# Performance work log

Measured on AMD Instinct MI355X. Metric: run time of the kernel, lower is better.

Reference implementation:

```python
import jax, jax.numpy as jnp
import numpy as np

SCALE = 0.25  # LoRA alpha / rank


def setup_inputs() -> dict:
    N, K, E, H, D, R = 1024, 2, 16, 1024, 2048, 16
    key = jax.random.key(0)
    ks = jax.random.split(key, 9)
    hidden_states = jax.random.normal(ks[0], (N, D), jnp.float32)
    topk_weights = jax.random.uniform(ks[1], (N, K), jnp.float32)
    topk_weights = topk_weights / topk_weights.sum(-1, keepdims=True)
    topk_ids = jax.random.randint(ks[2], (N, K), 0, E, jnp.int32)
    w_up = jax.random.normal(ks[3], (E, 2 * H, D), jnp.float32) * 0.02
    w_down = jax.random.normal(ks[4], (E, D, H), jnp.float32) * 0.02
    up_a = jax.random.normal(ks[5], (E, R, D), jnp.float32) * 0.02
    up_b = jax.random.normal(ks[6], (E, 2 * H, R), jnp.float32) * 0.02
    down_a = jax.random.normal(ks[7], (E, R, H), jnp.float32) * 0.02
    down_b = jax.random.normal(ks[8], (E, D, R), jnp.float32) * 0.02
    return {
        'hidden_states': hidden_states,
        'topk_weights': topk_weights,
        'topk_ids': topk_ids,
        'w_up': w_up,
        'w_down': w_down,
        'up_a': up_a,
        'up_b': up_b,
        'down_a': down_a,
        'down_b': down_b,
    }


def reference(hidden_states, topk_weights, topk_ids, w_up, w_down, up_a, up_b, down_a, down_b):
    H = w_down.shape[2]  # hidden_size
    # Up projection: dense per-expert GEMM, then gather the selected expert per (token, k).
    up_dense = jnp.einsum('nd,eod->neo', hidden_states, w_up)          # [N, E, 2H]
    up = jnp.take_along_axis(up_dense, topk_ids[:, :, None], axis=1)   # [N, K, 2H]
    # LoRA on up-proj: out[:, k] += (x @ A_e.T @ B_e.T) * scale
    t = jnp.einsum('nd,nkrd->nkr', hidden_states, up_a[topk_ids])      # [N, K, R]
    up = up + SCALE * jnp.einsum('nkr,nkor->nko', t, up_b[topk_ids])   # [N, K, 2H]
    # fused_gelu_and_mul: gelu(first half) * second half (erf gelu)
    act = jax.nn.gelu(up[..., :H], approximate=False) * up[..., H:]    # [N, K, H]
    # Down projection with routed-weight multiply.
    down_dense = jnp.einsum('nkh,edh->nked', act, w_down)              # [N, K, E, D]
    down = jnp.take_along_axis(down_dense, topk_ids[:, :, None, None], axis=2)[:, :, 0, :]  # [N, K, D]
    # LoRA on down-proj (topk_weights applied to lora path too, matching _apply_moe_lora)
    t2 = jnp.einsum('nkh,nkrh->nkr', act, down_a[topk_ids])            # [N, K, R]
    ldown = jnp.einsum('nkr,nkdr->nkd', t2, down_b[topk_ids])          # [N, K, D]
    down = (down + SCALE * ldown) * topk_weights[:, :, None]
    # moe_sum: reduce over top_k
    return down.sum(axis=1)                                            # [N, D]
```

## Files before the change

kernel.cpp:

```cpp
#include <hip/hip_runtime.h>
#include <math.h>

#define N_TOK 1024
#define TOPK  2
#define NEXP  16
#define HID   1024
#define DIM   2048
#define RANK  16
#define NPAIR (N_TOK * TOPK)
#define MOE_SCALE 0.25f
#define MAXTILES 31

typedef __attribute__((ext_vector_type(8))) short short8;
typedef __attribute__((ext_vector_type(4))) float floatx4;

static __device__ __forceinline__ unsigned short f2bf(float f) {
    union { float f; unsigned int u; } v; v.f = f;
    unsigned int u = v.u;
    u += 0x7fffu + ((u >> 16) & 1u);
    return (unsigned short)(u >> 16);
}

static __device__ __forceinline__ short8 cvt8(float4 a, float4 b) {
    short8 o;
    o[0] = (short)f2bf(a.x); o[1] = (short)f2bf(a.y);
    o[2] = (short)f2bf(a.z); o[3] = (short)f2bf(a.w);
    o[4] = (short)f2bf(b.x); o[5] = (short)f2bf(b.y);
    o[6] = (short)f2bf(b.z); o[7] = (short)f2bf(b.w);
    return o;
}

#define BAR() do { asm volatile("s_waitcnt lgkmcnt(0)" ::: "memory"); \
                   __builtin_amdgcn_s_barrier(); } while (0)

__global__ void k_routing(const int* __restrict__ ids,
                          int* __restrict__ offs,
                          int* __restrict__ sorted,
                          int* __restrict__ tlist,
                          int* __restrict__ tcount) {
    __shared__ int s_cnt[NEXP];
    __shared__ int s_off[NEXP + 1];
    int tid = threadIdx.x;
    if (tid < NEXP) s_cnt[tid] = 0;
    __syncthreads();
    for (int p = tid; p < NPAIR; p += blockDim.x) atomicAdd(&s_cnt[ids[p]], 1);
    __syncthreads();
    if (tid == 0) {
        int acc = 0;
        for (int e = 0; e < NEXP; ++e) { s_off[e] = acc; acc += s_cnt[e]; }
        s_off[NEXP] = acc;
        int t = 0;
        for (int e = 0; e < NEXP; ++e) {
            int c = s_off[e + 1] - s_off[e];
            for (int m = 0; m * 128 < c; ++m) tlist[t++] = (e << 8) | m;
        }
        *tcount = t;
    }
    __syncthreads();
    if (tid <= NEXP) offs[tid] = s_off[tid];
    if (tid < NEXP) s_cnt[tid] = s_off[tid];
    __syncthreads();
    for (int p = tid; p < NPAIR; p += blockDim.x) {
        int e = ids[p];
        int slot = atomicAdd(&s_cnt[e], 1);
        sorted[slot] = p;
    }
}

__global__ void k_cvt_x(const float* __restrict__ x, unsigned short* __restrict__ xbf) {
    size_t i = (size_t)blockIdx.x * blockDim.x + threadIdx.x;
    const float4* p = (const float4*)(x + i * 8);
    float4 a = p[0], b = p[1];
    *(short8*)(xbf + i * 8) = cvt8(a, b);
}

#define G_ISSUE(c, RA, RB, RU) do {                                          \
    const unsigned short* _a = aptr + (size_t)(c) * 64;                      \
    const float* _b = bptr + (size_t)(c) * 64;                               \
    _Pragma("unroll") for (int j = 0; j < 4; ++j)                            \
        RA[j] = *(const short8*)(_a + 8 * j);                                \
    _Pragma("unroll") for (int j = 0; j < 8; ++j)                            \
        RB[j] = *(const float4*)(_b + 4 * j);                                \
    if (tid < 128) {                                                         \
        const float* _u = uptr + (size_t)(c) * 64;                           \
        RU[0] = *(const float4*)_u;                                          \
        RU[1] = *(const float4*)(_u + 4);                                    \
    }                                                                        \
} while (0)

#define G_WRITE(RA, RB, RU, BUF) do {                                        \
    _Pragma("unroll") for (int cc = 0; cc < 4; ++cc) {                       \
        int cl = (tid & 1) * 4 + cc;                                         \
        *(short8*)(&sA[BUF][row * 64 + ((cl ^ (row & 7)) * 8)]) = RA[cc];    \
        short8 vb = cvt8(RB[2 * cc], RB[2 * cc + 1]);                        \
        *(short8*)(&sB[BUF][row * 64 + ((cl ^ (row & 7)) * 8)]) = vb;        \
    }                                                                        \
    if (tid < 128) {                                                         \
        short8 vu = cvt8(RU[0], RU[1]);                                      \
        int cl = tid & 7;                                                    \
        *(short8*)(&sU[BUF][urow * 64 + ((cl ^ (urow & 7)) * 8)]) = vu;      \
    }                                                                        \
} while (0)

#define G_MSTEP(BUF) do {                                                    \
    _Pragma("unroll") for (int kk = 0; kk < 2; ++kk) {                       \
        int r0 = wv * 32 + lm, r1 = wv * 32 + 16 + lm;                       \
        short8 af0 = *(const short8*)(&sA[BUF][r0 * 64 + (((kk * 4 + lq) ^ (r0 & 7)) * 8)]); \
        short8 af1 = *(const short8*)(&sA[BUF][r1 * 64 + (((kk * 4 + lq) ^ (r1 & 7)) * 8)]); \
        short8 uf  = *(const short8*)(&sU[BUF][lm * 64 + (((kk * 4 + lq) ^ (lm & 7)) * 8)]); \
        acct[0] = __builtin_amdgcn_mfma_f32_16x16x32_bf16(af0, uf, acct[0], 0, 0, 0); \
        acct[1] = __builtin_amdgcn_mfma_f32_16x16x32_bf16(af1, uf, acct[1], 0, 0, 0); \
        _Pragma("unroll") for (int n2 = 0; n2 < 8; ++n2) {                   \
            int rr = n2 * 16 + lm;                                           \
            short8 bf = *(const short8*)(&sB[BUF][rr * 64 + (((kk * 4 + lq) ^ (rr & 7)) * 8)]); \
            acc[0][n2] = __builtin_amdgcn_mfma_f32_16x16x32_bf16(af0, bf, acc[0][n2], 0, 0, 0); \
            acc[1][n2] = __builtin_amdgcn_mfma_f32_16x16x32_bf16(af1, bf, acc[1][n2], 0, 0, 0); \
        }                                                                    \
    }                                                                        \
} while (0)

#define G_PIPE(NC)                                                           \
    G_ISSUE(0, ra0, rb0, ru0);                                               \
    G_ISSUE(1, ra1, rb1, ru1);                                               \
    G_WRITE(ra0, rb0, ru0, 0);                                               \
    G_ISSUE(2, ra0, rb0, ru0);                                               \
    BAR();                                                                   \
    _Pragma("unroll 1")                                                      \
    for (int kc = 0; kc < (NC); kc += 2) {                                   \
        G_MSTEP(0);                                                          \
        G_WRITE(ra1, rb1, ru1, 1);                                           \
        if (kc + 3 < (NC)) G_ISSUE(kc + 3, ra1, rb1, ru1);                   \
        BAR();                                                               \
        G_MSTEP(1);                                                          \
        if (kc + 2 < (NC)) G_WRITE(ra0, rb0, ru0, 0);                        \
        if (kc + 4 < (NC)) G_ISSUE(kc + 4, ra0, rb0, ru0);                   \
        BAR();                                                               \
    }

__global__ __launch_bounds__(256, 2) void k_up(
        const unsigned short* __restrict__ xbf, const float* __restrict__ w_up,
        const float* __restrict__ up_a, const float* __restrict__ up_b,
        const int* __restrict__ offs, const int* __restrict__ sorted,
        const int* __restrict__ tlist, const int* __restrict__ tcount,
        unsigned short* __restrict__ act) {
    int wt = blockIdx.x;
    if (wt >= *tcount) return;
    int code = tlist[wt];
    int e = code >> 8, mt = code & 255;
    int nt = blockIdx.y;
    int off = offs[e], cnt = offs[e + 1] - off;

    __shared__ __align__(16) unsigned short sA[2][128 * 64];
    __shared__ __align__(16) unsigned short sB[2][128 * 64];
    __shared__ __align__(16) unsigned short sU[2][16 * 64];

    int tid = threadIdx.x, lane = tid & 63, wv = tid >> 6;
    int lm = lane & 15, lq = lane >> 4;

    int row  = tid >> 1;
    int colh = (tid & 1) * 32;

    int g = mt * 128 + row; if (g >= cnt) g = cnt - 1;
    int p = sorted[off + g];
    const unsigned short* aptr = xbf + (size_t)(p >> 1) * DIM + colh;

    int wrow = (row < 64) ? (nt * 64 + row) : (HID + nt * 64 + (row - 64));
    const float* bptr = w_up + ((size_t)e * 2 * HID + wrow) * DIM + colh;

    int urow = (tid >> 3) & 15, ucol = (tid & 7) * 8;
    const float* uptr = up_a + ((size_t)e * RANK + urow) * DIM + ucol;

    floatx4 zero = {0.f, 0.f, 0.f, 0.f};
    floatx4 acc[2][8], acct[2];
#pragma unroll
    for (int i = 0; i < 2; ++i) {
        acct[i] = zero;
#pragma unroll
        for (int j = 0; j < 8; ++j) acc[i][j] = zero;
    }

    short8 ra0[4], ra1[4];
    float4 rb0[8], rb1[8];
    float4 ru0[2], ru1[2];

    G_PIPE(32);

    float* t_s = (float*)&sA[0][0];
#pragma unroll
    for (int i = 0; i < 2; ++i)
#pragma unroll
        for (int j = 0; j < 4; ++j)
            t_s[(wv * 32 + i * 16 + lq * 4 + j) * 16 + lm] = MOE_SCALE * acct[i][j];
    BAR();

    const float* upb = up_b + (size_t)e * 2 * HID * RANK;
#pragma unroll
    for (int n2 = 0; n2 < 4; ++n2) {
        int h = nt * 64 + n2 * 16 + lm;
        const float* b1 = upb + (size_t)h * RANK;
        const float* b2 = upb + (size_t)(h + HID) * RANK;
        float r1[RANK], r2[RANK];
#pragma unroll
        for (int i = 0; i < RANK; ++i) { r1[i] = b1[i]; r2[i] = b2[i]; }
#pragma unroll
        for (int i = 0; i < 2; ++i) {
#pragma unroll
            for (int r = 0; r < 4; ++r) {
                int rl = wv * 32 + i * 16 + lq * 4 + r;
                int gg = mt * 128 + rl;
                if (gg < cnt) {
                    int slot = off + gg;
                    const float* tv = t_s + rl * 16;
                    float s1 = acc[i][n2][r], s2 = acc[i][n2 + 4][r];
#pragma unroll
                    for (int j = 0; j < RANK; ++j) { s1 += tv[j] * r1[j]; s2 += tv[j] * r2[j]; }
                    float gl = 0.5f * s1 * (1.f + erff(s1 * 0.70710678118654752f));
                    act[(size_t)slot * HID + h] = f2bf(gl * s2);
                }
            }
        }
    }
}

__global__ __launch_bounds__(256, 2) void k_down(
        const unsigned short* __restrict__ actg, const float* __restrict__ w_down,
        const float* __restrict__ tw, const float* __restrict__ down_a,
        const float* __restrict__ down_b,
        const int* __restrict__ offs, const int* __restrict__ sorted,
        const int* __restrict__ tlist, const int* __restrict__ tcount,
        float* __restrict__ out) {
    int wt = blockIdx.x;
    if (wt >= *tcount) return;
    int code = tlist[wt];
    int e = code >> 8, mt = code & 255;
    int nt = blockIdx.y;
    int off = offs[e], cnt = offs[e + 1] - off;

    __shared__ __align__(16) unsigned short sA[2][128 * 64];
    __shared__ __align__(16) unsigned short sB[2][128 * 64];
    __shared__ __align__(16) unsigned short sU[2][16 * 64];

    int tid = threadIdx.x, lane = tid & 63, wv = tid >> 6;
    int lm = lane & 15, lq = lane >> 4;

    int row  = tid >> 1;
    int colh = (tid & 1) * 32;

    int g = mt * 128 + row; if (g >= cnt) g = cnt - 1;
    const unsigned short* aptr = actg + (size_t)(off + g) * HID + colh;

    int d = nt * 128 + row;
    const float* bptr = w_down + ((size_t)e * DIM + d) * HID + colh;

    int urow = (tid >> 3) & 15, ucol = (tid & 7) * 8;
    const float* uptr = down_a + ((size_t)e * RANK + urow) * HID + ucol;

    floatx4 zero = {0.f, 0.f, 0.f, 0.f};
    floatx4 acc[2][8], acct[2];
#pragma unroll
    for (int i = 0; i < 2; ++i) {
        acct[i] = zero;
#pragma unroll
        for (int j = 0; j < 8; ++j) acc[i][j] = zero;
    }

    short8 ra0[4], ra1[4];
    float4 rb0[8], rb1[8];
    float4 ru0[2], ru1[2];

    G_PIPE(16);

    float* t_s = (float*)&sA[0][0];
#pragma unroll
    for (int i = 0; i < 2; ++i)
#pragma unroll
        for (int j = 0; j < 4; ++j)
            t_s[(wv * 32 + i * 16 + lq * 4 + j) * 16 + lm] = MOE_SCALE * acct[i][j];
    BAR();

#pragma unroll
    for (int n2 = 0; n2 < 8; ++n2) {
        int dd = nt * 128 + n2 * 16 + lm;
        const float* rb = down_b + ((size_t)e * DIM + dd) * RANK;
        float rbv[RANK];
#pragma unroll
        for (int i2 = 0; i2 < RANK; ++i2) rbv[i2] = rb[i2];
#pragma unroll
        for (int i = 0; i < 2; ++i) {
#pragma unroll
            for (int r = 0; r < 4; ++r) {
                int rl = wv * 32 + i * 16 + lq * 4 + r;
                int gg = mt * 128 + rl;
                if (gg < cnt) {
                    int slot = off + gg;
                    int pp = sorted[slot];
                    const float* tv = t_s + rl * 16;
                    float val = acc[i][n2][r];
#pragma unroll
                    for (int j = 0; j < RANK; ++j) val += tv[j] * rbv[j];
                    atomicAdd(&out[(size_t)(pp >> 1) * DIM + dd], val * tw[pp]);
                }
            }
        }
    }
}

extern "C" void kernel_launch(void* const* d_in, const int* in_sizes, int n_in,
                              void* d_out, int out_size, void* d_ws, size_t ws_size,
                              hipStream_t stream) {
    const float* x      = (const float*)d_in[0];
    const float* tw     = (const float*)d_in[1];
    const int*   ids    = (const int*)d_in[2];
    const float* w_up   = (const float*)d_in[3];
    const float* w_down = (const float*)d_in[4];
    const float* up_a   = (const float*)d_in[5];
    const float* up_b   = (const float*)d_in[6];
    const float* down_a = (const float*)d_in[7];
    const float* down_b = (const float*)d_in[8];
    float* out = (float*)d_out;

    char* ws = (char*)d_ws;
    int* offs   = (int*)ws;
    int* tlist  = (int*)(ws + 1024);
    int* tcount = (int*)(ws + 2048);
    int* sorted = (int*)(ws + 4096);
    unsigned short* act = (unsigned short*)(ws + 65536);
    unsigned short* xbf = (unsigned short*)(ws + 65536 + (size_t)NPAIR * HID * 2);

    hipMemsetAsync(d_out, 0, (size_t)out_size * sizeof(float), stream);

    k_routing<<<1, 256, 0, stream>>>(ids, offs, sorted, tlist, tcount);
    k_cvt_x<<<(N_TOK * DIM / 8 / 256), 256, 0, stream>>>(x, xbf);

    dim3 grid(MAXTILES, 16);
    k_up<<<grid, 256, 0, stream>>>(xbf, w_up, up_a, up_b, offs, sorted, tlist, tcount, act);
    k_down<<<grid, 256, 0, stream>>>(act, w_down, tw, down_a, down_b, offs, sorted, tlist, tcount, out);
}
```

Measured before the change: 603.4 us.

## Stream GEMM tiles into LDS with direct global-to-LDS loads, halve N tile

Replaces the register-staged global loads and LDS writes in both MoE GEMM kernels with direct global_load_lds transfers. Weights are now stored as fp32 in swizzled LDS and converted to bf16 at fragment-read time, and the pipeline waits on vmcnt counters instead of a register double buffer. The N tile shrinks from 128 to 64 columns, so the grid doubles to 32 column blocks. This aims to cut VGPR pressure and issue overhead in the load path. In exchange, each weight fragment is converted on every read, and the activation tile and LoRA-A are reloaded across twice as many blocks.

```diff
diff --git a/kernel.cpp b/kernel.cpp
--- a/kernel.cpp
+++ b/kernel.cpp
@@ -30,8 +30,19 @@
     return o;
 }
 
+static __device__ __forceinline__ short8 ldcvt(const float* base, int r, int c) {
+    float4 f0 = *(const float4*)(base + r * 64 + (((c)     ^ (r & 15)) * 4));
+    float4 f1 = *(const float4*)(base + r * 64 + (((c + 1) ^ (r & 15)) * 4));
+    return cvt8(f0, f1);
+}
+
 #define BAR() do { asm volatile("s_waitcnt lgkmcnt(0)" ::: "memory"); \
-                   __builtin_amdgcn_s_barrier(); } while (0)
+                   __builtin_amdgcn_s_barrier(); \
+                   asm volatile("" ::: "memory"); } while (0)
+
+#define GLDS16(G, L) __builtin_amdgcn_global_load_lds( \
+    (const __attribute__((address_space(1))) void*)(G), \
+    (__attribute__((address_space(3))) void*)(L), 16, 0, 0)
 
 __global__ void k_routing(const int* __restrict__ ids,
                           int* __restrict__ offs,
@@ -74,45 +85,25 @@
     *(short8*)(xbf + i * 8) = cvt8(a, b);
 }
 
-#define G_ISSUE(c, RA, RB, RU) do {                                          \
-    const unsigned short* _a = aptr + (size_t)(c) * 64;                      \
-    const float* _b = bptr + (size_t)(c) * 64;                               \
-    _Pragma("unroll") for (int j = 0; j < 4; ++j)                            \
-        RA[j] = *(const short8*)(_a + 8 * j);                                \
-    _Pragma("unroll") for (int j = 0; j < 8; ++j)                            \
-        RB[j] = *(const float4*)(_b + 4 * j);                                \
-    if (tid < 128) {                                                         \
-        const float* _u = uptr + (size_t)(c) * 64;                           \
-        RU[0] = *(const float4*)_u;                                          \
-        RU[1] = *(const float4*)(_u + 4);                                    \
-    }                                                                        \
-} while (0)
-
-#define G_WRITE(RA, RB, RU, BUF) do {                                        \
-    _Pragma("unroll") for (int cc = 0; cc < 4; ++cc) {                       \
-        int cl = (tid & 1) * 4 + cc;                                         \
-        *(short8*)(&sA[BUF][row * 64 + ((cl ^ (row & 7)) * 8)]) = RA[cc];    \
-        short8 vb = cvt8(RB[2 * cc], RB[2 * cc + 1]);                        \
-        *(short8*)(&sB[BUF][row * 64 + ((cl ^ (row & 7)) * 8)]) = vb;        \
-    }                                                                        \
-    if (tid < 128) {                                                         \
-        short8 vu = cvt8(RU[0], RU[1]);                                      \
-        int cl = tid & 7;                                                    \
-        *(short8*)(&sU[BUF][urow * 64 + ((cl ^ (urow & 7)) * 8)]) = vu;      \
-    }                                                                        \
+#define G_ISSUE(BUF) do {                                                    \
+    _Pragma("unroll") for (int i = 0; i < 4; ++i) {                          \
+        GLDS16(aq[i], &sA[BUF][(wv * 32 + 8 * i) * 64]); aq[i] += 64; }      \
+    _Pragma("unroll") for (int i = 0; i < 4; ++i) {                          \
+        GLDS16(bq[i], &sB[BUF][(wv * 16 + 4 * i) * 64]); bq[i] += 64; }      \
+    GLDS16(uq, &sU[BUF][(wv * 4) * 64]); uq += 64;                           \
 } while (0)
 
 #define G_MSTEP(BUF) do {                                                    \
     _Pragma("unroll") for (int kk = 0; kk < 2; ++kk) {                       \
-        int r0 = wv * 32 + lm, r1 = wv * 32 + 16 + lm;                       \
+        int r0 = wv * 32 + lm, r1 = r0 + 16;                                 \
         short8 af0 = *(const short8*)(&sA[BUF][r0 * 64 + (((kk * 4 + lq) ^ (r0 & 7)) * 8)]); \
         short8 af1 = *(const short8*)(&sA[BUF][r1 * 64 + (((kk * 4 + lq) ^ (r1 & 7)) * 8)]); \
-        short8 uf  = *(const short8*)(&sU[BUF][lm * 64 + (((kk * 4 + lq) ^ (lm & 7)) * 8)]); \
+        int c = kk * 8 + lq * 2;                                             \
+        short8 uf = ldcvt(&sU[BUF][0], lm, c);                               \
         acct[0] = __builtin_amdgcn_mfma_f32_16x16x32_bf16(af0, uf, acct[0], 0, 0, 0); \
         acct[1] = __builtin_amdgcn_mfma_f32_16x16x32_bf16(af1, uf, acct[1], 0, 0, 0); \
-        _Pragma("unroll") for (int n2 = 0; n2 < 8; ++n2) {                   \
-            int rr = n2 * 16 + lm;                                           \
-            short8 bf = *(const short8*)(&sB[BUF][rr * 64 + (((kk * 4 + lq) ^ (rr & 7)) * 8)]); \
+        _Pragma("unroll") for (int n2 = 0; n2 < 4; ++n2) {                   \
+            short8 bf = ldcvt(&sB[BUF][0], n2 * 16 + lm, c);                 \
             acc[0][n2] = __builtin_amdgcn_mfma_f32_16x16x32_bf16(af0, bf, acc[0][n2], 0, 0, 0); \
             acc[1][n2] = __builtin_amdgcn_mfma_f32_16x16x32_bf16(af1, bf, acc[1][n2], 0, 0, 0); \
         }                                                                    \
@@ -120,21 +111,18 @@
 } while (0)
 
 #define G_PIPE(NC)                                                           \
-    G_ISSUE(0, ra0, rb0, ru0);                                               \
-    G_ISSUE(1, ra1, rb1, ru1);                                               \
-    G_WRITE(ra0, rb0, ru0, 0);                                               \
-    G_ISSUE(2, ra0, rb0, ru0);                                               \
-    BAR();                                                                   \
+    G_ISSUE(0); G_ISSUE(1);                                                  \
     _Pragma("unroll 1")                                                      \
-    for (int kc = 0; kc < (NC); kc += 2) {                                   \
-        G_MSTEP(0);                                                          \
-        G_WRITE(ra1, rb1, ru1, 1);                                           \
-        if (kc + 3 < (NC)) G_ISSUE(kc + 3, ra1, rb1, ru1);                   \
-        BAR();                                                               \
-        G_MSTEP(1);                                                          \
-        if (kc + 2 < (NC)) G_WRITE(ra0, rb0, ru0, 0);                        \
-        if (kc + 4 < (NC)) G_ISSUE(kc + 4, ra0, rb0, ru0);                   \
-        BAR();                                                               \
+    for (int t = 0; t < (NC); ++t) {                                         \
+        if (t < (NC) - 1) asm volatile("s_waitcnt vmcnt(9)" ::: "memory");   \
+        else              asm volatile("s_waitcnt vmcnt(0)" ::: "memory");   \
+        __builtin_amdgcn_s_barrier();                                        \
+        asm volatile("" ::: "memory");                                       \
+        G_MSTEP(t & 1);                                                      \
+        asm volatile("s_waitcnt lgkmcnt(0)" ::: "memory");                   \
+        __builtin_amdgcn_s_barrier();                                        \
+        asm volatile("" ::: "memory");                                       \
+        if (t < (NC) - 2) G_ISSUE(t & 1);                                    \
     }
 
 __global__ __launch_bounds__(256, 2) void k_up(
@@ -151,37 +139,41 @@
     int off = offs[e], cnt = offs[e + 1] - off;
 
     __shared__ __align__(16) unsigned short sA[2][128 * 64];
-    __shared__ __align__(16) unsigned short sB[2][128 * 64];
-    __shared__ __align__(16) unsigned short sU[2][16 * 64];
+    __shared__ __align__(16) float          sB[2][64 * 64];
+    __shared__ __align__(16) float          sU[2][16 * 64];
 
     int tid = threadIdx.x, lane = tid & 63, wv = tid >> 6;
     int lm = lane & 15, lq = lane >> 4;
-
-    int row  = tid >> 1;
-    int colh = (tid & 1) * 32;
-
-    int g = mt * 128 + row; if (g >= cnt) g = cnt - 1;
-    int p = sorted[off + g];
-    const unsigned short* aptr = xbf + (size_t)(p >> 1) * DIM + colh;
-
-    int wrow = (row < 64) ? (nt * 64 + row) : (HID + nt * 64 + (row - 64));
-    const float* bptr = w_up + ((size_t)e * 2 * HID + wrow) * DIM + colh;
-
-    int urow = (tid >> 3) & 15, ucol = (tid & 7) * 8;
-    const float* uptr = up_a + ((size_t)e * RANK + urow) * DIM + ucol;
+    int l3 = lane >> 3, l7 = lane & 7, l4 = lane >> 4, l15 = lane & 15;
+
+    int acol = ((l7 ^ l3) * 8);
+    const unsigned short* aq[4];
+#pragma unroll
+    for (int i = 0; i < 4; ++i) {
+        int r = wv * 32 + 8 * i + l3;
+        int g = mt * 128 + r; if (g >= cnt) g = cnt - 1;
+        int p = sorted[off + g];
+        aq[i] = xbf + (size_t)(p >> 1) * DIM + acol;
+    }
+    const float* bq[4];
+#pragma unroll
+    for (int i = 0; i < 4; ++i) {
+        int tr = wv * 16 + 4 * i + l4;
+        int wrow = (tr < 32) ? (nt * 32 + tr) : (HID + nt * 32 + (tr - 32));
+        int bcol = ((l15 ^ (tr & 15)) * 4);
+        bq[i] = w_up + ((size_t)e * 2 * HID + wrow) * DIM + bcol;
+    }
+    int ur = wv * 4 + l4;
+    const float* uq = up_a + ((size_t)e * RANK + ur) * DIM + ((l15 ^ ur) * 4);
 
     floatx4 zero = {0.f, 0.f, 0.f, 0.f};
-    floatx4 acc[2][8], acct[2];
+    floatx4 acc[2][4], acct[2];
 #pragma unroll
     for (int i = 0; i < 2; ++i) {
         acct[i] = zero;
 #pragma unroll
-        for (int j = 0; j < 8; ++j) acc[i][j] = zero;
-    }
-
-    short8 ra0[4], ra1[4];
-    float4 rb0[8], rb1[8];
-    float4 ru0[2], ru1[2];
+        for (int j = 0; j < 4; ++j) acc[i][j] = zero;
+    }
 
     G_PIPE(32);
 
@@ -195,8 +187,8 @@
 
     const float* upb = up_b + (size_t)e * 2 * HID * RANK;
 #pragma unroll
-    for (int n2 = 0; n2 < 4; ++n2) {
-        int h = nt * 64 + n2 * 16 + lm;
+    for (int n2 = 0; n2 < 2; ++n2) {
+        int h = nt * 32 + n2 * 16 + lm;
         const float* b1 = upb + (size_t)h * RANK;
         const float* b2 = upb + (size_t)(h + HID) * RANK;
         float r1[RANK], r2[RANK];
@@ -211,7 +203,7 @@
                 if (gg < cnt) {
                     int slot = off + gg;
                     const float* tv = t_s + rl * 16;
-                    float s1 = acc[i][n2][r], s2 = acc[i][n2 + 4][r];
+                    float s1 = acc[i][n2][r], s2 = acc[i][n2 + 2][r];
 #pragma unroll
                     for (int j = 0; j < RANK; ++j) { s1 += tv[j] * r1[j]; s2 += tv[j] * r2[j]; }
                     float gl = 0.5f * s1 * (1.f + erff(s1 * 0.70710678118654752f));
@@ -237,36 +229,39 @@
     int off = offs[e], cnt = offs[e + 1] - off;
 
     __shared__ __align__(16) unsigned short sA[2][128 * 64];
-    __shared__ __align__(16) unsigned short sB[2][128 * 64];
-    __shared__ __align__(16) unsigned short sU[2][16 * 64];
+    __shared__ __align__(16) float          sB[2][64 * 64];
+    __shared__ __align__(16) float          sU[2][16 * 64];
 
     int tid = threadIdx.x, lane = tid & 63, wv = tid >> 6;
     int lm = lane & 15, lq = lane >> 4;
-
-    int row  = tid >> 1;
-    int colh = (tid & 1) * 32;
-
-    int g = mt * 128 + row; if (g >= cnt) g = cnt - 1;
-    const unsigned short* aptr = actg + (size_t)(off + g) * HID + colh;
-
-    int d = nt * 128 + row;
-    const float* bptr = w_down + ((size_t)e * DIM + d) * HID + colh;
-
-    int urow = (tid >> 3) & 15, ucol = (tid & 7) * 8;
-    const float* uptr = down_a + ((size_t)e * RANK + urow) * HID + ucol;
+    int l3 = lane >> 3, l7 = lane & 7, l4 = lane >> 4, l15 = lane & 15;
+
+    int acol = ((l7 ^ l3) * 8);
+    const unsigned short* aq[4];
+#pragma unroll
+    for (int i = 0; i < 4; ++i) {
+        int r = wv * 32 + 8 * i + l3;
+        int g = mt * 128 + r; if (g >= cnt) g = cnt - 1;
+        aq[i] = actg + (size_t)(off + g) * HID + acol;
+    }
+    const float* bq[4];
+#pragma unroll
+    for (int i = 0; i < 4; ++i) {
+        int tr = wv * 16 + 4 * i + l4;
+        int bcol = ((l15 ^ (tr & 15)) * 4);
+        bq[i] = w_down + ((size_t)e * DIM + nt * 64 + tr) * HID + bcol;
+    }
+    int ur = wv * 4 + l4;
+    const float* uq = down_a + ((size_t)e * RANK + ur) * HID + ((l15 ^ ur) * 4);
 
     floatx4 zero = {0.f, 0.f, 0.f, 0.f};
-    floatx4 acc[2][8], acct[2];
+    floatx4 acc[2][4], acct[2];
 #pragma unroll
     for (int i = 0; i < 2; ++i) {
         acct[i] = zero;
 #pragma unroll
-        for (int j = 0; j < 8; ++j) acc[i][j] = zero;
-    }
-
-    short8 ra0[4], ra1[4];
-    float4 rb0[8], rb1[8];
-    float4 ru0[2], ru1[2];
+        for (int j = 0; j < 4; ++j) acc[i][j] = zero;
+    }
 
     G_PIPE(16);
 
@@ -279,8 +274,8 @@
     BAR();
 
 #pragma unroll
-    for (int n2 = 0; n2 < 8; ++n2) {
-        int dd = nt * 128 + n2 * 16 + lm;
+    for (int n2 = 0; n2 < 4; ++n2) {
+        int dd = nt * 64 + n2 * 16 + lm;
         const float* rb = down_b + ((size_t)e * DIM + dd) * RANK;
         float rbv[RANK];
 #pragma unroll
@@ -332,7 +327,9 @@
     k_routing<<<1, 256, 0, stream>>>(ids, offs, sorted, tlist, tcount);
     k_cvt_x<<<(N_TOK * DIM / 8 / 256), 256, 0, stream>>>(x, xbf);
 
-    dim3 grid(MAXTILES, 16);
-    k_up<<<grid, 256, 0, stream>>>(xbf, w_up, up_a, up_b, offs, sorted, tlist, tcount, act);
-    k_down<<<grid, 256, 0, stream>>>(act, w_down, tw, down_a, down_b, offs, sorted, tlist, tcount, out);
-}
+    dim3 gup(MAXTILES, 32);
+    k_up<<<gup, 256, 0, stream>>>(xbf, w_up, up_a, up_b, offs, sorted, tlist, tcount, act);
+
+    dim3 gdn(MAXTILES, 32);
+    k_down<<<gdn, 256, 0, stream>>>(act, w_down, tw, down_a, down_b, offs, sorted, tlist, tcount, out);
+}
```

Measured after the change: 621.8 us. 1.03x slower.

## Pre-gather activations into MFMA fragment layout and drop LDS staging in GEMMs

Applied to the files above, without the earlier changes.

Replaces the x conversion kernel with a prep kernel that gathers routed tokens and writes bf16 x in a per-16-row MFMA fragment order. Both GEMMs now read A fragments directly from global memory and load fp32 weights straight into registers, converting them to bf16 there. This removes shared-memory tiling and barriers in the main loop, and the up kernel writes its output in the same fragment layout for the down kernel. Block tiles shrink in N (32 up, 64 down) and grids double, so each weight row is fetched without LDS reuse across waves, which raises global/L2 traffic in exchange for removing LDS round-trips and sync.

```diff
diff --git a/kernel.cpp b/kernel.cpp
--- a/kernel.cpp
+++ b/kernel.cpp
@@ -30,8 +30,8 @@
     return o;
 }
 
-#define BAR() do { asm volatile("s_waitcnt lgkmcnt(0)" ::: "memory"); \
-                   __builtin_amdgcn_s_barrier(); } while (0)
+#define XG_T16_STRIDE   (64 * 64 * 8)
+#define ACT_T16_STRIDE  (32 * 64 * 8)
 
 __global__ void k_routing(const int* __restrict__ ids,
                           int* __restrict__ offs,
@@ -67,82 +67,151 @@
     }
 }
 
-__global__ void k_cvt_x(const float* __restrict__ x, unsigned short* __restrict__ xbf) {
-    size_t i = (size_t)blockIdx.x * blockDim.x + threadIdx.x;
-    const float4* p = (const float4*)(x + i * 8);
-    float4 a = p[0], b = p[1];
-    *(short8*)(xbf + i * 8) = cvt8(a, b);
-}
-
-#define G_ISSUE(c, RA, RB, RU) do {                                          \
-    const unsigned short* _a = aptr + (size_t)(c) * 64;                      \
-    const float* _b = bptr + (size_t)(c) * 64;                               \
-    _Pragma("unroll") for (int j = 0; j < 4; ++j)                            \
-        RA[j] = *(const short8*)(_a + 8 * j);                                \
-    _Pragma("unroll") for (int j = 0; j < 8; ++j)                            \
-        RB[j] = *(const float4*)(_b + 4 * j);                                \
-    if (tid < 128) {                                                         \
-        const float* _u = uptr + (size_t)(c) * 64;                           \
-        RU[0] = *(const float4*)_u;                                          \
-        RU[1] = *(const float4*)(_u + 4);                                    \
+__global__ __launch_bounds__(256) void k_prep(
+        const float* __restrict__ x, const int* __restrict__ offs,
+        const int* __restrict__ sorted, const int* __restrict__ tlist,
+        const int* __restrict__ tcount, unsigned short* __restrict__ xg) {
+    int wt = blockIdx.x;
+    if (wt >= *tcount) return;
+    int code = tlist[wt];
+    int e = code >> 8, mt = code & 255;
+    int off = offs[e], cnt = offs[e + 1] - off;
+    int tid = threadIdx.x, lane = tid & 63, wv = tid >> 6;
+    int C = blockIdx.y * 4 + wv;
+    int r16 = lane & 15, lq = lane >> 4;
+#pragma unroll
+    for (int st = 0; st < 8; ++st) {
+        int g = mt * 128 + st * 16 + r16; if (g >= cnt) g = cnt - 1;
+        int tok = sorted[off + g] >> 1;
+        const float* src = x + (size_t)tok * DIM + C * 32 + lq * 8;
+        float4 a = *(const float4*)src;
+        float4 b = *(const float4*)(src + 4);
+        int T16 = wt * 8 + st;
+        *(short8*)(xg + (size_t)T16 * XG_T16_STRIDE + (size_t)(C * 64 + lane) * 8)
+            = cvt8(a, b);
+    }
+}
+
+#define LOADB2(t, B, P0, P1) do {                                            \
+    const float* _g = (P0) + (size_t)(t) * 64;                               \
+    const float* _m = (P1) + (size_t)(t) * 64;                               \
+    B[0] = *(const float4*)(_g);      B[1] = *(const float4*)(_g + 4);       \
+    B[2] = *(const float4*)(_g + 32); B[3] = *(const float4*)(_g + 36);      \
+    B[4] = *(const float4*)(_m);      B[5] = *(const float4*)(_m + 4);       \
+    B[6] = *(const float4*)(_m + 32); B[7] = *(const float4*)(_m + 36);      \
+} while (0)
+
+#define COMP(t, B, ACC0, ACC1) do {                                          \
+    short8 a0[4], a1[4];                                                     \
+    _Pragma("unroll") for (int mf = 0; mf < 4; ++mf) {                       \
+        a0[mf] = *(const short8*)(ap[mf] + (size_t)(2 * (t)) * 512);         \
+        a1[mf] = *(const short8*)(ap[mf] + (size_t)(2 * (t) + 1) * 512);     \
+    }                                                                        \
+    float4 u0a = *(const float4*)(uq + (size_t)(t) * 64);                    \
+    float4 u0b = *(const float4*)(uq + (size_t)(t) * 64 + 4);                \
+    float4 u1a = *(const float4*)(uq + (size_t)(t) * 64 + 32);               \
+    float4 u1b = *(const float4*)(uq + (size_t)(t) * 64 + 36);               \
+    short8 f00 = cvt8(B[0], B[1]), f01 = cvt8(B[2], B[3]);                   \
+    short8 f10 = cvt8(B[4], B[5]), f11 = cvt8(B[6], B[7]);                   \
+    short8 fu0 = cvt8(u0a, u0b),   fu1 = cvt8(u1a, u1b);                     \
+    _Pragma("unroll") for (int mf = 0; mf < 4; ++mf) {                       \
+        ACC0[mf] = __builtin_amdgcn_mfma_f32_16x16x32_bf16(a0[mf], f00, ACC0[mf], 0, 0, 0); \
+        ACC1[mf] = __builtin_amdgcn_mfma_f32_16x16x32_bf16(a0[mf], f10, ACC1[mf], 0, 0, 0); \
+        accT[mf] = __builtin_amdgcn_mfma_f32_16x16x32_bf16(a0[mf], fu0, accT[mf], 0, 0, 0); \
+        ACC0[mf] = __builtin_amdgcn_mfma_f32_16x16x32_bf16(a1[mf], f01, ACC0[mf], 0, 0, 0); \
+        ACC1[mf] = __builtin_amdgcn_mfma_f32_16x16x32_bf16(a1[mf], f11, ACC1[mf], 0, 0, 0); \
+        accT[mf] = __builtin_amdgcn_mfma_f32_16x16x32_bf16(a1[mf], fu1, accT[mf], 0, 0, 0); \
     }                                                                        \
 } while (0)
 
-#define G_WRITE(RA, RB, RU, BUF) do {                                        \
-    _Pragma("unroll") for (int cc = 0; cc < 4; ++cc) {                       \
-        int cl = (tid & 1) * 4 + cc;                                         \
-        *(short8*)(&sA[BUF][row * 64 + ((cl ^ (row & 7)) * 8)]) = RA[cc];    \
-        short8 vb = cvt8(RB[2 * cc], RB[2 * cc + 1]);                        \
-        *(short8*)(&sB[BUF][row * 64 + ((cl ^ (row & 7)) * 8)]) = vb;        \
-    }                                                                        \
-    if (tid < 128) {                                                         \
-        short8 vu = cvt8(RU[0], RU[1]);                                      \
-        int cl = tid & 7;                                                    \
-        *(short8*)(&sU[BUF][urow * 64 + ((cl ^ (urow & 7)) * 8)]) = vu;      \
-    }                                                                        \
-} while (0)
-
-#define G_MSTEP(BUF) do {                                                    \
-    _Pragma("unroll") for (int kk = 0; kk < 2; ++kk) {                       \
-        int r0 = wv * 32 + lm, r1 = wv * 32 + 16 + lm;                       \
-        short8 af0 = *(const short8*)(&sA[BUF][r0 * 64 + (((kk * 4 + lq) ^ (r0 & 7)) * 8)]); \
-        short8 af1 = *(const short8*)(&sA[BUF][r1 * 64 + (((kk * 4 + lq) ^ (r1 & 7)) * 8)]); \
-        short8 uf  = *(const short8*)(&sU[BUF][lm * 64 + (((kk * 4 + lq) ^ (lm & 7)) * 8)]); \
-        acct[0] = __builtin_amdgcn_mfma_f32_16x16x32_bf16(af0, uf, acct[0], 0, 0, 0); \
-        acct[1] = __builtin_amdgcn_mfma_f32_16x16x32_bf16(af1, uf, acct[1], 0, 0, 0); \
-        _Pragma("unroll") for (int n2 = 0; n2 < 8; ++n2) {                   \
-            int rr = n2 * 16 + lm;                                           \
-            short8 bf = *(const short8*)(&sB[BUF][rr * 64 + (((kk * 4 + lq) ^ (rr & 7)) * 8)]); \
-            acc[0][n2] = __builtin_amdgcn_mfma_f32_16x16x32_bf16(af0, bf, acc[0][n2], 0, 0, 0); \
-            acc[1][n2] = __builtin_amdgcn_mfma_f32_16x16x32_bf16(af1, bf, acc[1][n2], 0, 0, 0); \
+#define G_PIPE(NC, ACC0, ACC1)                                               \
+    {                                                                        \
+        float4 B0[8], B1[8];                                                 \
+        LOADB2(0, B0, bp0, bp1);                                             \
+        _Pragma("unroll 1")                                                  \
+        for (int t = 0; t + 2 < (NC); t += 2) {                              \
+            LOADB2(t + 1, B1, bp0, bp1);                                     \
+            COMP(t, B0, ACC0, ACC1);                                         \
+            LOADB2(t + 2, B0, bp0, bp1);                                     \
+            COMP(t + 1, B1, ACC0, ACC1);                                     \
         }                                                                    \
-    }                                                                        \
-} while (0)
-
-#define G_PIPE(NC)                                                           \
-    G_ISSUE(0, ra0, rb0, ru0);                                               \
-    G_ISSUE(1, ra1, rb1, ru1);                                               \
-    G_WRITE(ra0, rb0, ru0, 0);                                               \
-    G_ISSUE(2, ra0, rb0, ru0);                                               \
-    BAR();                                                                   \
-    _Pragma("unroll 1")                                                      \
-    for (int kc = 0; kc < (NC); kc += 2) {                                   \
-        G_MSTEP(0);                                                          \
-        G_WRITE(ra1, rb1, ru1, 1);                                           \
-        if (kc + 3 < (NC)) G_ISSUE(kc + 3, ra1, rb1, ru1);                   \
-        BAR();                                                               \
-        G_MSTEP(1);                                                          \
-        if (kc + 2 < (NC)) G_WRITE(ra0, rb0, ru0, 0);                        \
-        if (kc + 4 < (NC)) G_ISSUE(kc + 4, ra0, rb0, ru0);                   \
-        BAR();                                                               \
+        LOADB2((NC) - 1, B1, bp0, bp1);                                      \
+        COMP((NC) - 2, B0, ACC0, ACC1);                                      \
+        COMP((NC) - 1, B1, ACC0, ACC1);                                      \
     }
 
 __global__ __launch_bounds__(256, 2) void k_up(
-        const unsigned short* __restrict__ xbf, const float* __restrict__ w_up,
+        const unsigned short* __restrict__ xg, const float* __restrict__ w_up,
         const float* __restrict__ up_a, const float* __restrict__ up_b,
-        const int* __restrict__ offs, const int* __restrict__ sorted,
         const int* __restrict__ tlist, const int* __restrict__ tcount,
-        unsigned short* __restrict__ act) {
+        unsigned short* __restrict__ actg) {
+    int wt = blockIdx.x;
+    if (wt >= *tcount) return;
+    int code = tlist[wt];
+    int e = code >> 8;
+    int nt = blockIdx.y;
+
+    int tid = threadIdx.x, lane = tid & 63, wv = tid >> 6;
+    int tokg = wv & 1, hg = wv >> 1;
+    int lm = lane & 15, lq = lane >> 4;
+
+    const unsigned short* ap[4];
+#pragma unroll
+    for (int mf = 0; mf < 4; ++mf) {
+        int T16 = wt * 8 + tokg * 4 + mf;
+        ap[mf] = xg + (size_t)T16 * XG_T16_STRIDE + (size_t)lane * 8;
+    }
+    int h = nt * 32 + hg * 16 + lm;
+    const float* bp0 = w_up + ((size_t)e * 2 * HID + h) * DIM + lq * 8;
+    const float* bp1 = w_up + ((size_t)e * 2 * HID + HID + h) * DIM + lq * 8;
+    const float* uq  = up_a + ((size_t)e * RANK + lm) * DIM + lq * 8;
+
+    floatx4 zero = {0.f, 0.f, 0.f, 0.f};
+    floatx4 accG[4], accM[4], accT[4];
+#pragma unroll
+    for (int i = 0; i < 4; ++i) { accG[i] = zero; accM[i] = zero; accT[i] = zero; }
+
+    G_PIPE(32, accG, accM);
+
+    __shared__ float t_s[128 * 16];
+    if (wv < 2) {
+#pragma unroll
+        for (int mf = 0; mf < 4; ++mf)
+#pragma unroll
+            for (int j = 0; j < 4; ++j)
+                t_s[(tokg * 64 + mf * 16 + lq * 4 + j) * 16 + lm] = MOE_SCALE * accT[mf][j];
+    }
+    __syncthreads();
+
+    const float* b1 = up_b + ((size_t)e * 2 * HID + h) * RANK;
+    const float* b2 = up_b + ((size_t)e * 2 * HID + HID + h) * RANK;
+    float r1[RANK], r2[RANK];
+#pragma unroll
+    for (int i = 0; i < RANK; ++i) { r1[i] = b1[i]; r2[i] = b2[i]; }
+    int C = h >> 5, lsub = 16 * ((h >> 3) & 3), el = h & 7;
+#pragma unroll
+    for (int mf = 0; mf < 4; ++mf) {
+        int T16 = wt * 8 + tokg * 4 + mf;
+        unsigned short* dst = actg + (size_t)T16 * ACT_T16_STRIDE + (size_t)C * 512 + el;
+#pragma unroll
+        for (int r = 0; r < 4; ++r) {
+            int rl = tokg * 64 + mf * 16 + lq * 4 + r;
+            const float* tv = t_s + rl * 16;
+            float s1 = accG[mf][r], s2 = accM[mf][r];
+#pragma unroll
+            for (int j = 0; j < RANK; ++j) { s1 += tv[j] * r1[j]; s2 += tv[j] * r2[j]; }
+            float gl = 0.5f * s1 * (1.f + erff(s1 * 0.70710678118654752f));
+            dst[(size_t)(lq * 4 + r + lsub) * 8] = f2bf(gl * s2);
+        }
+    }
+}
+
+__global__ __launch_bounds__(256, 2) void k_down(
+        const unsigned short* __restrict__ actg, const float* __restrict__ w_down,
+        const float* __restrict__ tw, const float* __restrict__ down_a,
+        const float* __restrict__ down_b, const int* __restrict__ offs,
+        const int* __restrict__ sorted, const int* __restrict__ tlist,
+        const int* __restrict__ tcount, float* __restrict__ out) {
     int wt = blockIdx.x;
     if (wt >= *tcount) return;
     int code = tlist[wt];
@@ -150,156 +219,59 @@
     int nt = blockIdx.y;
     int off = offs[e], cnt = offs[e + 1] - off;
 
-    __shared__ __align__(16) unsigned short sA[2][128 * 64];
-    __shared__ __align__(16) unsigned short sB[2][128 * 64];
-    __shared__ __align__(16) unsigned short sU[2][16 * 64];
-
     int tid = threadIdx.x, lane = tid & 63, wv = tid >> 6;
+    int tokg = wv & 1, hg = wv >> 1;
     int lm = lane & 15, lq = lane >> 4;
 
-    int row  = tid >> 1;
-    int colh = (tid & 1) * 32;
-
-    int g = mt * 128 + row; if (g >= cnt) g = cnt - 1;
-    int p = sorted[off + g];
-    const unsigned short* aptr = xbf + (size_t)(p >> 1) * DIM + colh;
-
-    int wrow = (row < 64) ? (nt * 64 + row) : (HID + nt * 64 + (row - 64));
-    const float* bptr = w_up + ((size_t)e * 2 * HID + wrow) * DIM + colh;
-
-    int urow = (tid >> 3) & 15, ucol = (tid & 7) * 8;
-    const float* uptr = up_a + ((size_t)e * RANK + urow) * DIM + ucol;
+    const unsigned short* ap[4];
+#pragma unroll
+    for (int mf = 0; mf < 4; ++mf) {
+        int T16 = wt * 8 + tokg * 4 + mf;
+        ap[mf] = actg + (size_t)T16 * ACT_T16_STRIDE + (size_t)lane * 8;
+    }
+    int d0 = nt * 64 + hg * 32 + lm;
+    const float* bp0 = w_down + ((size_t)e * DIM + d0) * HID + lq * 8;
+    const float* bp1 = w_down + ((size_t)e * DIM + d0 + 16) * HID + lq * 8;
+    const float* uq  = down_a + ((size_t)e * RANK + lm) * HID + lq * 8;
 
     floatx4 zero = {0.f, 0.f, 0.f, 0.f};
-    floatx4 acc[2][8], acct[2];
-#pragma unroll
-    for (int i = 0; i < 2; ++i) {
-        acct[i] = zero;
-#pragma unroll
-        for (int j = 0; j < 8; ++j) acc[i][j] = zero;
-    }
-
-    short8 ra0[4], ra1[4];
-    float4 rb0[8], rb1[8];
-    float4 ru0[2], ru1[2];
-
-    G_PIPE(32);
-
-    float* t_s = (float*)&sA[0][0];
-#pragma unroll
-    for (int i = 0; i < 2; ++i)
-#pragma unroll
-        for (int j = 0; j < 4; ++j)
-            t_s[(wv * 32 + i * 16 + lq * 4 + j) * 16 + lm] = MOE_SCALE * acct[i][j];
-    BAR();
-
-    const float* upb = up_b + (size_t)e * 2 * HID * RANK;
-#pragma unroll
-    for (int n2 = 0; n2 < 4; ++n2) {
-        int h = nt * 64 + n2 * 16 + lm;
-        const float* b1 = upb + (size_t)h * RANK;
-        const float* b2 = upb + (size_t)(h + HID) * RANK;
-        float r1[RANK], r2[RANK];
-#pragma unroll
-        for (int i = 0; i < RANK; ++i) { r1[i] = b1[i]; r2[i] = b2[i]; }
-#pragma unroll
-        for (int i = 0; i < 2; ++i) {
-#pragma unroll
-            for (int r = 0; r < 4; ++r) {
-                int rl = wv * 32 + i * 16 + lq * 4 + r;
-                int gg = mt * 128 + rl;
-                if (gg < cnt) {
-                    int slot = off + gg;
-                    const float* tv = t_s + rl * 16;
-                    float s1 = acc[i][n2][r], s2 = acc[i][n2 + 4][r];
-#pragma unroll
-                    for (int j = 0; j < RANK; ++j) { s1 += tv[j] * r1[j]; s2 += tv[j] * r2[j]; }
-                    float gl = 0.5f * s1 * (1.f + erff(s1 * 0.70710678118654752f));
-                    act[(size_t)slot * HID + h] = f2bf(gl * s2);
-                }
-            }
-        }
-    }
-}
-
-__global__ __launch_bounds__(256, 2) void k_down(
-        const unsigned short* __restrict__ actg, const float* __restrict__ w_down,
-        const float* __restrict__ tw, const float* __restrict__ down_a,
-        const float* __restrict__ down_b,
-        const int* __restrict__ offs, const int* __restrict__ sorted,
-        const int* __restrict__ tlist, const int* __restrict__ tcount,
-        float* __restrict__ out) {
-    int wt = blockIdx.x;
-    if (wt >= *tcount) return;
-    int code = tlist[wt];
-    int e = code >> 8, mt = code & 255;
-    int nt = blockIdx.y;
-    int off = offs[e], cnt = offs[e + 1] - off;
-
-    __shared__ __align__(16) unsigned short sA[2][128 * 64];
-    __shared__ __align__(16) unsigned short sB[2][128 * 64];
-    __shared__ __align__(16) unsigned short sU[2][16 * 64];
-
-    int tid = threadIdx.x, lane = tid & 63, wv = tid >> 6;
-    int lm = lane & 15, lq = lane >> 4;
-
-    int row  = tid >> 1;
-    int colh = (tid & 1) * 32;
-
-    int g = mt * 128 + row; if (g >= cnt) g = cnt - 1;
-    const unsigned short* aptr = actg + (size_t)(off + g) * HID + colh;
-
-    int d = nt * 128 + row;
-    const float* bptr = w_down + ((size_t)e * DIM + d) * HID + colh;
-
-    int urow = (tid >> 3) & 15, ucol = (tid & 7) * 8;
-    const float* uptr = down_a + ((size_t)e * RANK + urow) * HID + ucol;
-
-    floatx4 zero = {0.f, 0.f, 0.f, 0.f};
-    floatx4 acc[2][8], acct[2];
-#pragma unroll
-    for (int i = 0; i < 2; ++i) {
-        acct[i] = zero;
-#pragma unroll
-        for (int j = 0; j < 8; ++j) acc[i][j] = zero;
-    }
-
-    short8 ra0[4], ra1[4];
-    float4 rb0[8], rb1[8];
-    float4 ru0[2], ru1[2];
-
-    G_PIPE(16);
-
-    float* t_s = (float*)&sA[0][0];
-#pragma unroll
-    for (int i = 0; i < 2; ++i)
-#pragma unroll
-        for (int j = 0; j < 4; ++j)
-            t_s[(wv * 32 + i * 16 + lq * 4 + j) * 16 + lm] = MOE_SCALE * acct[i][j];
-    BAR();
-
-#pragma unroll
-    for (int n2 = 0; n2 < 8; ++n2) {
-        int dd = nt * 128 + n2 * 16 + lm;
-        const float* rb = down_b + ((size_t)e * DIM + dd) * RANK;
-        float rbv[RANK];
-#pragma unroll
-        for (int i2 = 0; i2 < RANK; ++i2) rbv[i2] = rb[i2];
-#pragma unroll
-        for (int i = 0; i < 2; ++i) {
-#pragma unroll
-            for (int r = 0; r < 4; ++r) {
-                int rl = wv * 32 + i * 16 + lq * 4 + r;
-                int gg = mt * 128 + rl;
-                if (gg < cnt) {
-                    int slot = off + gg;
-                    int pp = sorted[slot];
-                    const float* tv = t_s + rl * 16;
-                    float val = acc[i][n2][r];
-#pragma unroll
-                    for (int j = 0; j < RANK; ++j) val += tv[j] * rbv[j];
-                    atomicAdd(&out[(size_t)(pp >> 1) * DIM + dd], val * tw[pp]);
-                }
+    floatx4 acc0[4], acc1[4], accT[4];
+#pragma unroll
+    for (int i = 0; i < 4; ++i) { acc0[i] = zero; acc1[i] = zero; accT[i] = zero; }
+
+    G_PIPE(16, acc0, acc1);
+
+    __shared__ float t_s[128 * 16];
+    if (wv < 2) {
+#pragma unroll
+        for (int mf = 0; mf < 4; ++mf)
+#pragma unroll
+            for (int j = 0; j < 4; ++j)
+                t_s[(tokg * 64 + mf * 16 + lq * 4 + j) * 16 + lm] = MOE_SCALE * accT[mf][j];
+    }
+    __syncthreads();
+
+    const float* q0 = down_b + ((size_t)e * DIM + d0) * RANK;
+    const float* q1 = down_b + ((size_t)e * DIM + d0 + 16) * RANK;
+    float rb0[RANK], rb1[RANK];
+#pragma unroll
+    for (int i = 0; i < RANK; ++i) { rb0[i] = q0[i]; rb1[i] = q1[i]; }
+#pragma unroll
+    for (int mf = 0; mf < 4; ++mf) {
+#pragma unroll
+        for (int r = 0; r < 4; ++r) {
+            int rl = tokg * 64 + mf * 16 + lq * 4 + r;
+            int gg = mt * 128 + rl;
+            if (gg < cnt) {
+                int pp = sorted[off + gg];
+                const float* tv = t_s + rl * 16;
+                float v0 = acc0[mf][r], v1 = acc1[mf][r];
+#pragma unroll
+                for (int j = 0; j < RANK; ++j) { v0 += tv[j] * rb0[j]; v1 += tv[j] * rb1[j]; }
+                float w = tw[pp];
+                float* op = out + (size_t)(pp >> 1) * DIM;
+                atomicAdd(op + d0, v0 * w);
+                atomicAdd(op + d0 + 16, v1 * w);
             }
         }
     }
@@ -324,15 +296,19 @@
     int* tlist  = (int*)(ws + 1024);
     int* tcount = (int*)(ws + 2048);
     int* sorted = (int*)(ws + 4096);
-    unsigned short* act = (unsigned short*)(ws + 65536);
-    unsigned short* xbf = (unsigned short*)(ws + 65536 + (size_t)NPAIR * HID * 2);
+    unsigned short* xg   = (unsigned short*)(ws + 65536);
+    unsigned short* actg = (unsigned short*)(ws + 65536 + (size_t)MAXTILES * 8 * XG_T16_STRIDE * 2);
 
     hipMemsetAsync(d_out, 0, (size_t)out_size * sizeof(float), stream);
 
     k_routing<<<1, 256, 0, stream>>>(ids, offs, sorted, tlist, tcount);
-    k_cvt_x<<<(N_TOK * DIM / 8 / 256), 256, 0, stream>>>(x, xbf);
-
-    dim3 grid(MAXTILES, 16);
-    k_up<<<grid, 256, 0, stream>>>(xbf, w_up, up_a, up_b, offs, sorted, tlist, tcount, act);
-    k_down<<<grid, 256, 0, stream>>>(act, w_down, tw, down_a, down_b, offs, sorted, tlist, tcount, out);
-}
+
+    dim3 gprep(MAXTILES, 16);
+    k_prep<<<gprep, 256, 0, stream>>>(x, offs, sorted, tlist, tcount, xg);
+
+    dim3 gup(MAXTILES, 32);
+    k_up<<<gup, 256, 0, stream>>>(xg, w_up, up_a, up_b, tlist, tcount, actg);
+
+    dim3 gdn(MAXTILES, 32);
+    k_down<<<gdn, 256, 0, stream>>>(actg, w_down, tw, down_a, down_b, offs, sorted, tlist, tcount, out);
+}
```

New measurement: 728.3 us. 1.21x slower.
